# Performance work log

Measured on AMD Instinct MI355X. Metric: run time of the kernel, lower is better.

Reference implementation:

```python
import jax, jax.numpy as jnp
import numpy as np

BETA = 0.9
THR = 1.0  # snn.Leaky default threshold
H = 250
OUT = 2


def setup_inputs() -> dict:
    key = jax.random.key(0)
    ks = jax.random.split(key, 7)
    T, B, N = 1000, 512, 128
    x = jax.random.normal(ks[0], (T, B, N), dtype=jnp.float32)

    def linear_init(kw, kb, fan_in, fan_out):
        s = 1.0 / np.sqrt(fan_in)
        W = jax.random.uniform(kw, (fan_in, fan_out), jnp.float32, -s, s)
        b = jax.random.uniform(kb, (fan_out,), jnp.float32, -s, s)
        return W, b

    W1, b1 = linear_init(ks[1], ks[2], N, H)
    W2, b2 = linear_init(ks[3], ks[4], H, H)
    W3, b3 = linear_init(ks[5], ks[6], H, OUT)
    return {"x": x, "W1": W1, "b1": b1, "W2": W2, "b2": b2, "W3": W3, "b3": b3}


def reference(x, W1, b1, W2, b2, W3, b3):
    # snnTorch Leaky (reset_mechanism='subtract'):
    #   reset   = (mem_prev > thr)            (detached)
    #   mem_new = beta*mem_prev + cur - reset*thr
    #   spk     = (mem_new > thr)
    def lif(mem, cur):
        reset = (mem > THR).astype(cur.dtype)
        mem = BETA * mem + cur - reset * THR
        spk = (mem > THR).astype(cur.dtype)
        return mem, spk

    B = x.shape[1]
    dt = x.dtype

    def step(carry, xt):
        m1, m2, m3 = carry
        m1, s1 = lif(m1, xt @ W1 + b1)   # [B, 250]
        m2, s2 = lif(m2, s1 @ W2 + b2)   # [B, 250]
        m3, s3 = lif(m3, s2 @ W3 + b3)   # [B, 2]
        return (m1, m2, m3), (s3, m3)

    init = (jnp.zeros((B, H), dt), jnp.zeros((B, H), dt), jnp.zeros((B, OUT), dt))
    _, (spikes, mem_rec) = jax.lax.scan(step, init, x)
    return spikes, mem_rec  # each [T, B, 2]
```

## Files before the change

kernel.cpp:

```cpp
#include <hip/hip_runtime.h>
#include <cstdint>

#define HID 250
#define NIN 128
#define BATCH 512
#define N1 (BATCH * HID)
#define T_TOTAL 1000
#define OUT_HALF 1024000

__global__ __launch_bounds__(256) void pad_w(
    const float* __restrict__ W1, const float* __restrict__ W2,
    float* __restrict__ W1p, float* __restrict__ W2p)
{
    const int i = blockIdx.x * 256 + threadIdx.x;
    if (i < 128 * 256) {
        const int k = i >> 8, c = i & 255;
        W1p[i] = (c < HID) ? W1[k * HID + c] : 0.0f;
    }
    if (i < 250 * 256) {
        const int k = i >> 8, c = i & 255;
        W2p[i] = (c < HID) ? W2[k * HID + c] : 0.0f;
    }
}

__global__ __launch_bounds__(256, 2) void gemm1_v4(
    const float* __restrict__ x,
    const float* __restrict__ W1p,
    const float* __restrict__ b1,
    float* __restrict__ cur,
    int M)
{
#pragma clang fp contract(off)
    __shared__ __align__(16) float xT[128 * 132];
    const int tid  = threadIdx.x;
    const int lane = tid & 63, wave = tid >> 6;
    const long rowBase = (long)blockIdx.x * 128;

    const float* xb = x + rowBase * NIN;
    #pragma unroll
    for (int i = 0; i < 16; ++i) {
        const int rr  = i & 1;
        const int kq  = (i >> 1) * 4 + wave;
        const int row = rr * 64 + lane;
        const float4 v = *(const float4*)(xb + (long)row * NIN + kq * 4);
        xT[(4 * kq + 0) * 132 + row] = v.x;
        xT[(4 * kq + 1) * 132 + row] = v.y;
        xT[(4 * kq + 2) * 132 + row] = v.z;
        xT[(4 * kq + 3) * 132 + row] = v.w;
    }
    __syncthreads();

    const int ri = tid >> 4;
    const int ci = tid & 15;

    float acc[8][16];
    #pragma unroll
    for (int r = 0; r < 8; ++r)
        #pragma unroll
        for (int c = 0; c < 16; ++c) acc[r][c] = 0.0f;

    #pragma unroll 2
    for (int k = 0; k < NIN; ++k) {
        const float4 a0 = *(const float4*)&xT[k * 132 + 8 * ri];
        const float4 a1 = *(const float4*)&xT[k * 132 + 8 * ri + 4];
        const float* wr = W1p + (k << 8) + 4 * ci;
        const float4 wv0 = *(const float4*)(wr);
        const float4 wv1 = *(const float4*)(wr + 64);
        const float4 wv2 = *(const float4*)(wr + 128);
        const float4 wv3 = *(const float4*)(wr + 192);
        const float w[16] = {wv0.x, wv0.y, wv0.z, wv0.w,
                             wv1.x, wv1.y, wv1.z, wv1.w,
                             wv2.x, wv2.y, wv2.z, wv2.w,
                             wv3.x, wv3.y, wv3.z, wv3.w};
        const float av[8] = {a0.x, a0.y, a0.z, a0.w, a1.x, a1.y, a1.z, a1.w};
        #pragma unroll
        for (int r = 0; r < 8; ++r)
            #pragma unroll
            for (int c = 0; c < 16; ++c)
                acc[r][c] = __builtin_fmaf(av[r], w[c], acc[r][c]);
    }

    #pragma unroll
    for (int j = 0; j < 4; ++j) {
        #pragma unroll
        for (int p = 0; p < 2; ++p) {
            const int cp = 64 * j + 4 * ci + 2 * p;
            if (cp < HID) {
                const float b0 = b1[cp], b1v = b1[cp + 1];
                #pragma unroll
                for (int r = 0; r < 8; ++r) {
                    const long row = rowBase + 8 * ri + r;
                    float2 o;
                    o.x = acc[r][4*j + 2*p]     + b0;
                    o.y = acc[r][4*j + 2*p + 1] + b1v;
                    *(float2*)(cur + row * HID + cp) = o;
                }
            }
        }
    }
}

__global__ __launch_bounds__(256) void scan_f32(
    const float* __restrict__ cur,
    uint8_t* __restrict__ spk,
    float* __restrict__ state,
    int Tc)
{
#pragma clang fp contract(off)
    const int n = blockIdx.x * 256 + threadIdx.x;
    float m = state[n];
    int t = 0;
    for (; t + 8 <= Tc; t += 8) {
        const long base = (long)t * N1 + n;
        float c[8];
        #pragma unroll
        for (int u = 0; u < 8; ++u) c[u] = cur[base + (long)u * N1];
        #pragma unroll
        for (int u = 0; u < 8; ++u) {
            const float r = (m > 1.0f) ? 1.0f : 0.0f;
            float tmp = 0.9f * m; tmp = tmp + c[u]; m = tmp - r;
            spk[base + (long)u * N1] = (m > 1.0f) ? (uint8_t)1 : (uint8_t)0;
        }
    }
    for (; t < Tc; ++t) {
        const long base = (long)t * N1 + n;
        const float c = cur[base];
        const float r = (m > 1.0f) ? 1.0f : 0.0f;
        float tmp = 0.9f * m; tmp = tmp + c; m = tmp - r;
        spk[base] = (m > 1.0f) ? (uint8_t)1 : (uint8_t)0;
    }
    state[n] = m;
}

__global__ __launch_bounds__(512, 4) void gemm2_v4(
    const uint8_t* __restrict__ s,
    const float* __restrict__ W2p,
    const float* __restrict__ b2,
    float* __restrict__ cur,
    int M)
{
#pragma clang fp contract(off)
    __shared__ __align__(16) float Wq[250 * 32];
    const int tid  = threadIdx.x;
    const int lane = tid & 63, wave = tid >> 6;
    const int q    = blockIdx.x & 7;
    const long r0  = (long)(blockIdx.x >> 3) * 128;
    const int c32  = lane & 31;
    const int half = lane >> 5;

    {
        const float* src = W2p + q * 32;
        #pragma unroll
        for (int i = 0; i < 4; ++i) {
            const int idx = i * 512 + tid;
            if (idx < 2000) {
                const int k = idx >> 3, c4 = (idx & 7) * 4;
                *(float4*)&Wq[k * 32 + c4] = *(const float4*)(src + k * 256 + c4);
            }
        }
    }
    const int col = q * 32 + c32;
    const float bb = (col < HID) ? b2[col] : 0.0f;
    __syncthreads();

    for (int p = 0; p < 8; ++p) {
        const long ra = r0 + wave * 16 + 2 * p;
        const long rb = ra + 1;
        const uint8_t* pa = s + ra * HID;
        const uint8_t* pb = s + rb * HID;
        unsigned long long ma[4], mb[4];
        #pragma unroll
        for (int c = 0; c < 4; ++c) {
            const int k = c * 64 + lane;
            ma[c] = __ballot((k < HID) && pa[k]);
            mb[c] = __ballot((k < HID) && pb[k]);
        }
        float acc = 0.0f;
        #pragma unroll
        for (int c = 0; c < 4; ++c) {
            unsigned long long mu = ma[c] | mb[c];
            const unsigned long long msel = half ? mb[c] : ma[c];
            while (mu) {
                const int k = __builtin_ctzll(mu);
                mu &= mu - 1;
                const float wv = Wq[(c * 64 + k) * 32 + c32];
                acc = acc + (((msel >> k) & 1ull) ? wv : 0.0f);
            }
        }
        const long row = half ? rb : ra;
        if (col < HID) cur[row * HID + col] = acc + bb;
    }
}

__global__ __launch_bounds__(256) void gemm3_f32(
    const uint8_t* __restrict__ s,
    const float* __restrict__ W3,
    const float* __restrict__ b3,
    float* __restrict__ cur3,
    int M)
{
#pragma clang fp contract(off)
    __shared__ int wl[4][256];
    const int tid = threadIdx.x;
    const int wave = tid >> 6, lane = tid & 63;
    const long row = (long)blockIdx.x * 4 + wave;

    int base = 0;
    #pragma unroll
    for (int c = 0; c < 4; ++c) {
        const int k = c * 64 + lane;
        const bool sp = (k < HID) && s[row * HID + k];
        unsigned long long mask = __ballot(sp);
        if (sp) wl[wave][base + __popcll(mask & ((1ull << lane) - 1ull))] = k;
        base += __popcll(mask);
    }
    __syncthreads();

    if (lane < 2) {
        const int nact = base;
        float acc = 0.0f;
        for (int j = 0; j < nact; ++j)
            acc = acc + W3[wl[wave][j] * 2 + lane];
        cur3[row * 2 + lane] = acc + b3[lane];
    }
}

__global__ __launch_bounds__(256) void scan3_f32(
    const float* __restrict__ cur3,
    float* __restrict__ state,
    float* __restrict__ out,
    int t0, int Tc)
{
#pragma clang fp contract(off)
    const int n = blockIdx.x * 256 + threadIdx.x;
    float m = state[n];
    int t = 0;
    for (; t + 8 <= Tc; t += 8) {
        float c[8];
        #pragma unroll
        for (int u = 0; u < 8; ++u) c[u] = cur3[(long)(t + u) * 1024 + n];
        #pragma unroll
        for (int u = 0; u < 8; ++u) {
            const float reset = (m > 1.0f) ? 1.0f : 0.0f;
            float tmp = 0.9f * m; tmp = tmp + c[u]; m = tmp - reset;
            const long o = (long)(t0 + t + u) * 1024 + n;
            out[o] = (m > 1.0f) ? 1.0f : 0.0f;
            out[OUT_HALF + o] = m;
        }
    }
    for (; t < Tc; ++t) {
        const float c = cur3[(long)t * 1024 + n];
        const float reset = (m > 1.0f) ? 1.0f : 0.0f;
        float tmp = 0.9f * m; tmp = tmp + c; m = tmp - reset;
        const long o = (long)(t0 + t) * 1024 + n;
        out[o] = (m > 1.0f) ? 1.0f : 0.0f;
        out[OUT_HALF + o] = m;
    }
    state[n] = m;
}

extern "C" void kernel_launch(void* const* d_in, const int* in_sizes, int n_in,
                              void* d_out, int out_size, void* d_ws, size_t ws_size,
                              hipStream_t stream) {
    const float* x  = (const float*)d_in[0];
    const float* W1 = (const float*)d_in[1];
    const float* b1 = (const float*)d_in[2];
    const float* W2 = (const float*)d_in[3];
    const float* b2 = (const float*)d_in[4];
    const float* W3 = (const float*)d_in[5];
    const float* b3 = (const float*)d_in[6];
    float* out = (float*)d_out;

    char* w = (char*)d_ws;
    size_t off = 0;
    auto alloc = [&](size_t bytes) -> void* {
        void* p = (void*)(w + off);
        off = (off + bytes + 255) & ~(size_t)255;
        return p;
    };

    float* m1 = (float*)alloc((size_t)N1 * 4);
    float* m2 = (float*)alloc((size_t)N1 * 4);
    float* m3 = (float*)alloc(1024 * 4);
    const size_t states = off;
    float* W1p = (float*)alloc(128 * 256 * 4);
    float* W2p = (float*)alloc(250 * 256 * 4);
    const size_t fixed = off;

    const size_t perT = 4096 + 128000 + 512000;
    long tc_budget = ((long)ws_size - (long)fixed - 4096) / (long)perT;
    int Tc = (int)(tc_budget < 1 ? 1 : (tc_budget > T_TOTAL ? T_TOTAL : tc_budget));

    float*   cur3 = (float*)alloc((size_t)Tc * 4096);
    uint8_t* sbuf = (uint8_t*)alloc((size_t)Tc * 128000);
    float*   cur  = (float*)alloc((size_t)Tc * 512000);

    hipMemsetAsync(d_ws, 0, states, stream);
    pad_w<<<250, 256, 0, stream>>>(W1, W2, W1p, W2p);

    for (int t0 = 0; t0 < T_TOTAL; t0 += Tc) {
        const int tc = (T_TOTAL - t0 < Tc) ? (T_TOTAL - t0) : Tc;
        const int M = tc * BATCH;

        gemm1_v4<<<M / 128, 256, 0, stream>>>(x + (size_t)t0 * BATCH * NIN,
                                              W1p, b1, cur, M);
        scan_f32<<<N1 / 256, 256, 0, stream>>>(cur, sbuf, m1, tc);
        gemm2_v4<<<(M / 128) * 8, 512, 0, stream>>>(sbuf, W2p, b2, cur, M);
        scan_f32<<<N1 / 256, 256, 0, stream>>>(cur, sbuf, m2, tc);
        gemm3_f32<<<M / 4, 256, 0, stream>>>(sbuf, W3, b3, cur3, M);
        scan3_f32<<<4, 256, 0, stream>>>(cur3, m3, out, t0, tc);
    }
}
```

Baseline: 2.189 ms.

## Replace sparse ballot-based spike GEMM with dense packed-FMA LDS-staged GEMM

Layer-2 GEMM changes from walking ballot masks of spiking inputs per row pair to a dense formulation. Each wave stages 8 rows of spikes as floats in LDS and accumulates all 250 inputs with v_pk_fma_f32, 8 rows per lane. Weight tiles widen to 64 columns and are loaded with global_load_lds, so the grid has 4 column blocks of 512 rows each. The goal is to remove the data-dependent serial spike loops and wave divergence. In exchange the kernel does fixed dense work regardless of sparsity and uses about 160KB of LDS, which limits it to one block per CU.

```diff
diff --git a/kernel.cpp b/kernel.cpp
--- a/kernel.cpp
+++ b/kernel.cpp
@@ -7,6 +7,8 @@
 #define N1 (BATCH * HID)
 #define T_TOTAL 1000
 #define OUT_HALF 1024000
+
+typedef float f32x2 __attribute__((ext_vector_type(2)));
 
 __global__ __launch_bounds__(256) void pad_w(
     const float* __restrict__ W1, const float* __restrict__ W2,
@@ -132,7 +134,7 @@
     state[n] = m;
 }
 
-__global__ __launch_bounds__(512, 4) void gemm2_v4(
+__global__ __launch_bounds__(512, 1) void gemm2_v5(
     const uint8_t* __restrict__ s,
     const float* __restrict__ W2p,
     const float* __restrict__ b2,
@@ -140,55 +142,80 @@
     int M)
 {
 #pragma clang fp contract(off)
-    __shared__ __align__(16) float Wq[250 * 32];
+    __shared__ __align__(16) float Wq[250 * 64];
+    __shared__ __align__(16) float stab[8 * 250 * 12];
     const int tid  = threadIdx.x;
     const int lane = tid & 63, wave = tid >> 6;
-    const int q    = blockIdx.x & 7;
-    const long r0  = (long)(blockIdx.x >> 3) * 128;
-    const int c32  = lane & 31;
-    const int half = lane >> 5;
+    const int q    = blockIdx.x & 3;
+    const long rb  = (long)(blockIdx.x >> 2) * 512;
 
     {
-        const float* src = W2p + q * 32;
-        #pragma unroll
-        for (int i = 0; i < 4; ++i) {
+        const float* src = W2p + q * 64;
+        #pragma unroll
+        for (int i = 0; i < 8; ++i) {
             const int idx = i * 512 + tid;
-            if (idx < 2000) {
-                const int k = idx >> 3, c4 = (idx & 7) * 4;
-                *(float4*)&Wq[k * 32 + c4] = *(const float4*)(src + k * 256 + c4);
+            if (idx < 4000) {
+                const int k = idx >> 4, c4 = (idx & 15) * 4;
+                __builtin_amdgcn_global_load_lds(
+                    (const __attribute__((address_space(1))) uint32_t*)(src + k * 256 + c4),
+                    (__attribute__((address_space(3))) uint32_t*)&Wq[idx * 4],
+                    16, 0, 0);
             }
         }
     }
-    const int col = q * 32 + c32;
+    const int col = q * 64 + lane;
     const float bb = (col < HID) ? b2[col] : 0.0f;
     __syncthreads();
 
-    for (int p = 0; p < 8; ++p) {
-        const long ra = r0 + wave * 16 + 2 * p;
-        const long rb = ra + 1;
-        const uint8_t* pa = s + ra * HID;
-        const uint8_t* pb = s + rb * HID;
-        unsigned long long ma[4], mb[4];
+    float* stw = stab + wave * (250 * 12);
+    const float* wq_l = Wq + lane;
+    float* stw_l = stw + lane * 12;
+
+    for (int g = 0; g < 8; ++g) {
+        const long grow = rb + (long)wave * 64 + g * 8;
+        const uint8_t* sp = s + grow * HID;
+
         #pragma unroll
         for (int c = 0; c < 4; ++c) {
-            const int k = c * 64 + lane;
-            ma[c] = __ballot((k < HID) && pa[k]);
-            mb[c] = __ballot((k < HID) && pb[k]);
-        }
-        float acc = 0.0f;
-        #pragma unroll
-        for (int c = 0; c < 4; ++c) {
-            unsigned long long mu = ma[c] | mb[c];
-            const unsigned long long msel = half ? mb[c] : ma[c];
-            while (mu) {
-                const int k = __builtin_ctzll(mu);
-                mu &= mu - 1;
-                const float wv = Wq[(c * 64 + k) * 32 + c32];
-                acc = acc + (((msel >> k) & 1ull) ? wv : 0.0f);
+            uint32_t by[8];
+            #pragma unroll
+            for (int r = 0; r < 8; ++r)
+                by[r] = sp[r * HID + c * 64 + lane];
+            if (c < 3 || lane < 58) {
+                #pragma unroll
+                for (int p = 0; p < 4; ++p) {
+                    f32x2 sv;
+                    sv.x = (float)by[2 * p];
+                    sv.y = (float)by[2 * p + 1];
+                    *(f32x2*)(stw_l + c * 768 + 2 * p) = sv;
+                }
             }
         }
-        const long row = half ? rb : ra;
-        if (col < HID) cur[row * HID + col] = acc + bb;
+
+        f32x2 a0 = {0.0f, 0.0f}, a1 = {0.0f, 0.0f};
+        f32x2 a2 = {0.0f, 0.0f}, a3 = {0.0f, 0.0f};
+        const f32x2* st2 = (const f32x2*)stw;
+        #pragma unroll 50
+        for (int k = 0; k < HID; ++k) {
+            const float w = wq_l[k * 64];
+            f32x2 wd; wd.x = w; wd.y = w;
+            const f32x2 s0 = st2[k * 6 + 0];
+            const f32x2 s1 = st2[k * 6 + 1];
+            const f32x2 s2 = st2[k * 6 + 2];
+            const f32x2 s3 = st2[k * 6 + 3];
+            asm("v_pk_fma_f32 %0, %1, %2, %0" : "+v"(a0) : "v"(s0), "v"(wd));
+            asm("v_pk_fma_f32 %0, %1, %2, %0" : "+v"(a1) : "v"(s1), "v"(wd));
+            asm("v_pk_fma_f32 %0, %1, %2, %0" : "+v"(a2) : "v"(s2), "v"(wd));
+            asm("v_pk_fma_f32 %0, %1, %2, %0" : "+v"(a3) : "v"(s3), "v"(wd));
+        }
+
+        if (col < HID) {
+            float* cp = cur + grow * HID + col;
+            cp[0 * HID] = a0.x + bb;  cp[1 * HID] = a0.y + bb;
+            cp[2 * HID] = a1.x + bb;  cp[3 * HID] = a1.y + bb;
+            cp[4 * HID] = a2.x + bb;  cp[5 * HID] = a2.y + bb;
+            cp[6 * HID] = a3.x + bb;  cp[7 * HID] = a3.y + bb;
+        }
     }
 }
 
@@ -305,7 +332,7 @@
         gemm1_v4<<<M / 128, 256, 0, stream>>>(x + (size_t)t0 * BATCH * NIN,
                                               W1p, b1, cur, M);
         scan_f32<<<N1 / 256, 256, 0, stream>>>(cur, sbuf, m1, tc);
-        gemm2_v4<<<(M / 128) * 8, 512, 0, stream>>>(sbuf, W2p, b2, cur, M);
+        gemm2_v5<<<(M / 512) * 4, 512, 0, stream>>>(sbuf, W2p, b2, cur, M);
         scan_f32<<<N1 / 256, 256, 0, stream>>>(cur, sbuf, m2, tc);
         gemm3_f32<<<M / 4, 256, 0, stream>>>(sbuf, W3, b3, cur3, M);
         scan3_f32<<<4, 256, 0, stream>>>(cur3, m3, out, t0, tc);
```

New measurement: 2.870 ms. +31.1%, slower.
